# Kernel optimization log

Measured on AMD Instinct MI355X. Metric: run time of the kernel, lower is better.

Reference implementation:

```python
import jax, jax.numpy as jnp
import numpy as np

# Faithful JAX port of the approxmatch EMD kernel (Fan et al.) wrapped by emdDist.
# 10 soft-assignment (auction-style) iterations with annealed temperature level=-4^j,
# j = 7..-1, final iteration level = 0. match is accumulated transport mass;
# cost[b] = sum_{k,l} match[b,k,l] * ||x1_k - x2_l||.

_EPS = 1e-9


def _approxmatch(xyz1, xyz2):
    # xyz1: (b, n, 3), xyz2: (b, m, 3)
    b, n, _ = xyz1.shape
    m = xyz2.shape[1]
    factorl = max(n, m) / n
    factorr = max(n, m) / m
    remainL = jnp.full((b, n), factorl, dtype=xyz1.dtype)   # mass left on xyz1 points
    remainR = jnp.full((b, m), factorr, dtype=xyz1.dtype)   # capacity left on xyz2 points
    # pairwise squared distances (b, n, m)
    d2 = jnp.sum((xyz1[:, :, None, :] - xyz2[:, None, :, :]) ** 2, axis=-1)
    match = jnp.zeros((b, n, m), dtype=xyz1.dtype)
    for j in range(7, -3, -1):  # j = 7, 6, ..., -1, -2
        level = 0.0 if j == -2 else -(4.0 ** j)
        # proposal weights from each left point, scaled by remaining right capacity
        w = jnp.exp(level * d2) * remainR[:, None, :]                      # (b,n,m)
        w = w / (jnp.sum(w, axis=-1, keepdims=True) + _EPS) * remainL[:, :, None]
        # right points accept at most their remaining capacity
        sumr = jnp.sum(w, axis=1) + _EPS                                   # (b,m)
        ratio = jnp.minimum(remainR / sumr, 1.0)                           # (b,m)
        delta = w * ratio[:, None, :]                                      # accepted transfer
        match = match + delta
        remainL = jnp.maximum(remainL - jnp.sum(delta, axis=-1), 0.0)
        remainR = jnp.maximum(remainR - jnp.sum(delta, axis=1), 0.0)
    return match, d2


def setup_inputs() -> dict:
    key = jax.random.key(0)
    k1, k2 = jax.random.split(key)
    B, N, M = 8, 4096, 4096
    input1 = jax.random.normal(k1, (B, N, 3), dtype=jnp.float32)
    input2 = jax.random.normal(k2, (B, M, 3), dtype=jnp.float32)
    return {"input1": input1, "input2": input2}


def reference(input1, input2):
    match, d2 = _approxmatch(input1, input2)
    # original CUDA backward treats match as a constant -> stop_gradient
    match = jax.lax.stop_gradient(match)
    dist = jnp.sqrt(jnp.maximum(d2, 1e-12))
    cost = jnp.sum(match * dist, axis=(1, 2))  # (b,)
    return cost
```

## Files before the change

### kernel.cpp

```cpp
#include <hip/hip_runtime.h>

#define NPTS 4096
#define NB   8
#define TPB  256
#define TPBR 128
#define MBLK 4
#define EPSC 1e-9f

#define EXP2(x)  __builtin_amdgcn_exp2f(x)
#define RCPF(x)  __builtin_amdgcn_rcpf(x)
#define SQRTF(x) __builtin_amdgcn_sqrtf(x)

template<int MODE, bool SKIP, int CHUNK>
__global__ __launch_bounds__(TPB) void ca_kernel(
    const float* __restrict__ x2,
    float* __restrict__ dbufP,
    float* __restrict__ rsumP,
    const float* __restrict__ x1,
    const float* __restrict__ ubuf,
    const float* __restrict__ rrbuf,
    float* __restrict__ out, float sc)
{
  __shared__ float4 x2s[CHUNK];
  __shared__ float  rrs[CHUNK];

  const int tid = threadIdx.x;
  const int nchunk = blockIdx.x, mseg = blockIdx.y, b = blockIdx.z;
  const int m0 = mseg * CHUNK;

  if (MODE == 0 && nchunk == 0 && mseg == 0 && tid == 0) out[b] = 0.f;

  for (int mm = tid; mm < CHUNK; mm += TPB) {
    int m = m0 + mm;
    const float* q = x2 + ((size_t)b * NPTS + m) * 3;
    float u = 0.f, rrn = 1.f;
    if (MODE >= 1) { u = ubuf[b * NPTS + m]; rrn = rrbuf[b * NPTS + m]; }
    x2s[mm] = make_float4(sc * q[0], sc * q[1], sc * q[2], u);
    rrs[mm] = rrn;
  }
  __syncthreads();

  const int n0 = nchunk * (TPB * MBLK) + tid;
  float px[MBLK], py[MBLK], pz[MBLK], dacc[MBLK], racc[MBLK];
#pragma unroll
  for (int k = 0; k < MBLK; ++k) {
    const float* p = x1 + ((size_t)b * NPTS + n0 + k * TPB) * 3;
    px[k] = sc * p[0]; py[k] = sc * p[1]; pz[k] = sc * p[2];
    dacc[k] = 0.f; racc[k] = 0.f;
  }

#pragma unroll 4
  for (int mm = 0; mm < CHUNK; ++mm) {
    float4 q  = x2s[mm];
    float rrv = rrs[mm];
    float ds2[MBLK];
#pragma unroll
    for (int k = 0; k < MBLK; ++k) {
      float dx = px[k] - q.x, dy = py[k] - q.y, dz = pz[k] - q.z;
      ds2[k] = fmaf(dz, dz, fmaf(dy, dy, dx * dx));
    }
    if (MODE == 2) {
#pragma unroll
      for (int k = 0; k < MBLK; ++k) {
        dacc[k] += rrv;
        float ec = EXP2(-ds2[k]);
        racc[k] = fmaf(ec, q.w, racc[k]);
      }
    } else {
      bool go = true;
      if (SKIP) {
        float dmin = ds2[0];
#pragma unroll
        for (int k = 1; k < MBLK; ++k) dmin = fminf(dmin, ds2[k]);
        go = dmin < 126.f;
      }
      if (go) {
#pragma unroll
        for (int k = 0; k < MBLK; ++k) {
          float en = EXP2(-ds2[k]);
          dacc[k] = fmaf(en, rrv, dacc[k]);
          if (MODE == 1) { float e2 = en * en; racc[k] = fmaf(e2 * e2, q.w, racc[k]); }
        }
      }
    }
  }

  size_t base = ((size_t)mseg * NB + b) * NPTS;
#pragma unroll
  for (int k = 0; k < MBLK; ++k) {
    dbufP[base + n0 + k * TPB] = dacc[k];
    if (MODE >= 1) rsumP[base + n0 + k * TPB] = racc[k];
  }
}

template<int LVL0, bool SKIP, int CHUNK>
__global__ __launch_bounds__(TPB) void b_kernel(
    const float* __restrict__ x1,
    const float* __restrict__ abuf,
    float* __restrict__ s0P, float* __restrict__ s1P,
    const float* __restrict__ x2, float sc, float inv_s)
{
  __shared__ float4 x1s[CHUNK];

  const int tid = threadIdx.x;
  const int mchunk = blockIdx.x, nsegi = blockIdx.y, b = blockIdx.z;
  const int n0 = nsegi * CHUNK;

  for (int nn = tid; nn < CHUNK; nn += TPB) {
    int n = n0 + nn;
    const float* p = x1 + ((size_t)b * NPTS + n) * 3;
    float a = abuf[b * NPTS + n];
    x1s[nn] = make_float4(sc * p[0], sc * p[1], sc * p[2], a);
  }
  __syncthreads();

  const int m0 = mchunk * (TPB * MBLK) + tid;
  float qx[MBLK], qy[MBLK], qz[MBLK], s0a[MBLK], s1a[MBLK];
#pragma unroll
  for (int k = 0; k < MBLK; ++k) {
    const float* q = x2 + ((size_t)b * NPTS + m0 + k * TPB) * 3;
    qx[k] = sc * q[0]; qy[k] = sc * q[1]; qz[k] = sc * q[2];
    s0a[k] = 0.f; s1a[k] = 0.f;
  }

#pragma unroll 4
  for (int nn = 0; nn < CHUNK; ++nn) {
    float4 p = x1s[nn];
    float ds2[MBLK];
#pragma unroll
    for (int k = 0; k < MBLK; ++k) {
      float dx = p.x - qx[k], dy = p.y - qy[k], dz = p.z - qz[k];
      ds2[k] = fmaf(dz, dz, fmaf(dy, dy, dx * dx));
    }
    if (LVL0) {
#pragma unroll
      for (int k = 0; k < MBLK; ++k) {
        s0a[k] += p.w;
        s1a[k] = fmaf(p.w, SQRTF(ds2[k]), s1a[k]);
      }
    } else {
      bool go = true;
      if (SKIP) {
        float dmin = ds2[0];
#pragma unroll
        for (int k = 1; k < MBLK; ++k) dmin = fminf(dmin, ds2[k]);
        go = dmin < 126.f;
      }
      if (go) {
#pragma unroll
        for (int k = 0; k < MBLK; ++k) {
          float e  = EXP2(-ds2[k]);
          float tt = p.w * e;
          s0a[k] += tt;
          s1a[k] = fmaf(tt, SQRTF(ds2[k]), s1a[k]);
        }
      }
    }
  }

  size_t base = ((size_t)nsegi * NB + b) * NPTS;
#pragma unroll
  for (int k = 0; k < MBLK; ++k) {
    s0P[base + m0 + k * TPB] = s0a[k];
    s1P[base + m0 + k * TPB] = s1a[k] * inv_s;
  }
}

template<int NSEG>
__global__ __launch_bounds__(TPBR) void r1_kernel(
    const float* __restrict__ dbufP, const float* __restrict__ rsumP,
    float* __restrict__ lbuf, float* __restrict__ dtot,
    float* __restrict__ abuf, int iter)
{
  const int idx = blockIdx.x * TPBR + threadIdx.x;
  const int b = idx >> 12, n = idx & (NPTS - 1);
  const int off = b * NPTS + n;

  float dnew = 0.f;
#pragma unroll
  for (int s = 0; s < NSEG; ++s) dnew += dbufP[((size_t)s * NB + b) * NPTS + n];

  float rl;
  if (iter == 0) {
    rl = 1.f;
  } else {
    float rlp = lbuf[off];
    float ap  = rlp * RCPF(dtot[off] + EPSC);
    float rs = 0.f;
#pragma unroll
    for (int s = 0; s < NSEG; ++s) rs += rsumP[((size_t)s * NB + b) * NPTS + n];
    rl = fmaxf(rlp - ap * rs, 0.f);
  }
  lbuf[off] = rl;
  dtot[off] = dnew;
  abuf[off] = rl * RCPF(dnew + EPSC);
}

template<int NSEG, bool LAST>
__global__ __launch_bounds__(TPBR) void r2_kernel(
    const float* __restrict__ s0P, const float* __restrict__ s1P,
    float* __restrict__ ubuf, float* __restrict__ rrbuf,
    float* __restrict__ out, int iter)
{
  __shared__ float red[TPBR];
  const int idx = blockIdx.x * TPBR + threadIdx.x;
  const int b = idx >> 12, m = idx & (NPTS - 1);
  const int off = b * NPTS + m;

  float s0 = 0.f, s1 = 0.f;
#pragma unroll
  for (int s = 0; s < NSEG; ++s) {
    s0 += s0P[((size_t)s * NB + b) * NPTS + m];
    s1 += s1P[((size_t)s * NB + b) * NPTS + m];
  }
  float rr    = (iter == 0) ? 1.f : rrbuf[off];
  float sumr  = fmaf(rr, s0, EPSC);
  float ratio = fminf(rr * RCPF(sumr), 1.f);
  float u     = rr * ratio;
  if (!LAST) {
    ubuf[off]  = u;
    rrbuf[off] = fmaxf(rr - u * s0, 0.f);
  }

  red[threadIdx.x] = u * s1;
  __syncthreads();
  for (int s = TPBR / 2; s > 0; s >>= 1) {
    if (threadIdx.x < s) red[threadIdx.x] += red[threadIdx.x + s];
    __syncthreads();
  }
  if (threadIdx.x == 0) atomicAdd(out + b, red[0]);
}

template<int NSEG>
static void run_all(const float* x1, const float* x2, float* out, float* ws,
                    hipStream_t stream)
{
  constexpr int CHUNK = NPTS / NSEG;
  const size_t plane = (size_t)NB * NPTS;

  float* dbufP = ws;
  float* rsumP = dbufP + (size_t)NSEG * plane;
  float* s0P   = rsumP + (size_t)NSEG * plane;
  float* s1P   = s0P   + (size_t)NSEG * plane;
  float* dtot  = s1P   + (size_t)NSEG * plane;
  float* lbuf  = dtot  + plane;
  float* abuf  = lbuf  + plane;
  float* ubuf  = abuf  + plane;
  float* rrbuf = ubuf  + plane;

  const double L2E = 1.4426950408889634074;
  const double lv[10] = {-16384.0, -4096.0, -1024.0, -256.0, -64.0,
                         -16.0, -4.0, -1.0, -0.25, 0.0};
  float scl[10], inv_s[10];
  for (int i = 0; i < 10; ++i) {
    double c2 = lv[i] * L2E;
    scl[i]   = (i == 9) ? 1.f : (float)sqrt(-c2);
    inv_s[i] = (i == 9) ? 1.f : (float)(1.0 / sqrt(-c2));
  }

  dim3 gmain(NPTS / (TPB * MBLK), NSEG, NB), bmain(TPB);
  dim3 gr(NPTS * NB / TPBR), br(TPBR);

  ca_kernel<0, true, CHUNK><<<gmain, bmain, 0, stream>>>(
      x2, dbufP, rsumP, x1, ubuf, rrbuf, out, scl[0]);

  for (int i = 0; i < 10; ++i) {
    r1_kernel<NSEG><<<gr, br, 0, stream>>>(dbufP, rsumP, lbuf, dtot, abuf, i);

    if (i <= 2)
      b_kernel<0, true, CHUNK><<<gmain, bmain, 0, stream>>>(
          x1, abuf, s0P, s1P, x2, scl[i], inv_s[i]);
    else if (i <= 8)
      b_kernel<0, false, CHUNK><<<gmain, bmain, 0, stream>>>(
          x1, abuf, s0P, s1P, x2, scl[i], inv_s[i]);
    else
      b_kernel<1, false, CHUNK><<<gmain, bmain, 0, stream>>>(
          x1, abuf, s0P, s1P, x2, 1.f, 1.f);

    if (i < 9)
      r2_kernel<NSEG, false><<<gr, br, 0, stream>>>(s0P, s1P, ubuf, rrbuf, out, i);
    else
      r2_kernel<NSEG, true><<<gr, br, 0, stream>>>(s0P, s1P, ubuf, rrbuf, out, i);

    if (i <= 7) {
      if (i <= 1)
        ca_kernel<1, true, CHUNK><<<gmain, bmain, 0, stream>>>(
            x2, dbufP, rsumP, x1, ubuf, rrbuf, out, scl[i + 1]);
      else
        ca_kernel<1, false, CHUNK><<<gmain, bmain, 0, stream>>>(
            x2, dbufP, rsumP, x1, ubuf, rrbuf, out, scl[i + 1]);
    } else if (i == 8) {
      ca_kernel<2, false, CHUNK><<<gmain, bmain, 0, stream>>>(
          x2, dbufP, rsumP, x1, ubuf, rrbuf, out, scl[8]);
    }
  }
}

extern "C" void kernel_launch(void* const* d_in, const int* in_sizes, int n_in,
                              void* d_out, int out_size, void* d_ws, size_t ws_size,
                              hipStream_t stream) {
  const float* x1 = (const float*)d_in[0];
  const float* x2 = (const float*)d_in[1];
  float* out = (float*)d_out;
  float* ws  = (float*)d_ws;

  const size_t plane = (size_t)NB * NPTS;
  auto need = [&](int nseg) {
    return ((size_t)(4 * nseg + 5) * plane) * sizeof(float);
  };

  if (ws_size >= need(64))      run_all<64>(x1, x2, out, ws, stream);
  else if (ws_size >= need(32)) run_all<32>(x1, x2, out, ws, stream);
  else                          run_all<16>(x1, x2, out, ws, stream);
}
```

Baseline: 1.034 ms.

## Morton-sort point clouds to make far-distance tile skipping effective

Adds a per-batch counting sort of both point sets by a coarse Morton code so spatially nearby points share tiles, letting the wavefront-level skip test (min distance above threshold) fire far more often; the skip path is extended to more iterations. Distances are rewritten in the |p|^2+|q|^2-2pq form, points are stored as float4, the u/rr buffers are packed into float2, and outputs use vectorised stores. Partial-sum buffers are aliased between phases to cut workspace. The cost is an extra sort kernel and possible cancellation error in the expanded distance form, partly guarded by taking abs before the sqrt.

```diff
diff --git a/kernel.cpp b/kernel.cpp
--- a/kernel.cpp
+++ b/kernel.cpp
@@ -11,159 +11,204 @@
 #define RCPF(x)  __builtin_amdgcn_rcpf(x)
 #define SQRTF(x) __builtin_amdgcn_sqrtf(x)
 
+__global__ __launch_bounds__(TPB) void sort_kernel(
+    const float* __restrict__ x1, const float* __restrict__ x2,
+    float4* __restrict__ x1p, float4* __restrict__ x2p)
+{
+  __shared__ unsigned int   hist[4096];
+  __shared__ unsigned short codes[4096];
+  __shared__ unsigned int   part[TPB];
+
+  const int set = blockIdx.x, b = blockIdx.y;
+  const float* src = set ? x2 : x1;
+  float4* dst = set ? x2p : x1p;
+  const int tid = threadIdx.x;
+
+  for (int i = tid; i < 4096; i += TPB) hist[i] = 0;
+  __syncthreads();
+
+  for (int j = 0; j < NPTS / TPB; ++j) {
+    int n = j * TPB + tid;
+    const float* p = src + ((size_t)b * NPTS + n) * 3;
+    float x = p[0], y = p[1], z = p[2];
+    int qx = min(max((int)((x + 4.f) * 2.f), 0), 15);
+    int qy = min(max((int)((y + 4.f) * 2.f), 0), 15);
+    int qz = min(max((int)((z + 4.f) * 2.f), 0), 15);
+    auto ex = [](int v) {
+      return (v & 1) | ((v & 2) << 2) | ((v & 4) << 4) | ((v & 8) << 6);
+    };
+    int code = ex(qx) | (ex(qy) << 1) | (ex(qz) << 2);
+    codes[n] = (unsigned short)code;
+    atomicAdd(&hist[code], 1u);
+  }
+  __syncthreads();
+
+  unsigned int loc[16], s = 0;
+#pragma unroll
+  for (int j = 0; j < 16; ++j) { loc[j] = s; s += hist[tid * 16 + j]; }
+  part[tid] = s;
+  __syncthreads();
+  if (tid == 0) {
+    unsigned int run = 0;
+    for (int t = 0; t < TPB; ++t) { unsigned int v = part[t]; part[t] = run; run += v; }
+  }
+  __syncthreads();
+  {
+    unsigned int base = part[tid];
+#pragma unroll
+    for (int j = 0; j < 16; ++j) hist[tid * 16 + j] = base + loc[j];
+  }
+  __syncthreads();
+
+  for (int j = 0; j < NPTS / TPB; ++j) {
+    int n = j * TPB + tid;
+    const float* p = src + ((size_t)b * NPTS + n) * 3;
+    float x = p[0], y = p[1], z = p[2];
+    unsigned int pos = atomicAdd(&hist[codes[n]], 1u);
+    dst[(size_t)b * NPTS + pos] = make_float4(x, y, z, 0.f);
+  }
+}
+
 template<int MODE, bool SKIP, int CHUNK>
 __global__ __launch_bounds__(TPB) void ca_kernel(
-    const float* __restrict__ x2,
-    float* __restrict__ dbufP,
-    float* __restrict__ rsumP,
-    const float* __restrict__ x1,
-    const float* __restrict__ ubuf,
-    const float* __restrict__ rrbuf,
+    const float4* __restrict__ x2p, const float4* __restrict__ x1p,
+    const float2* __restrict__ urP,
+    float* __restrict__ dbufP, float* __restrict__ rsumP,
     float* __restrict__ out, float sc)
 {
   __shared__ float4 x2s[CHUNK];
-  __shared__ float  rrs[CHUNK];
+  __shared__ float2 urs[CHUNK];
 
   const int tid = threadIdx.x;
   const int nchunk = blockIdx.x, mseg = blockIdx.y, b = blockIdx.z;
-  const int m0 = mseg * CHUNK;
 
   if (MODE == 0 && nchunk == 0 && mseg == 0 && tid == 0) out[b] = 0.f;
 
   for (int mm = tid; mm < CHUNK; mm += TPB) {
-    int m = m0 + mm;
-    const float* q = x2 + ((size_t)b * NPTS + m) * 3;
-    float u = 0.f, rrn = 1.f;
-    if (MODE >= 1) { u = ubuf[b * NPTS + m]; rrn = rrbuf[b * NPTS + m]; }
-    x2s[mm] = make_float4(sc * q[0], sc * q[1], sc * q[2], u);
-    rrs[mm] = rrn;
-  }
-  __syncthreads();
-
-  const int n0 = nchunk * (TPB * MBLK) + tid;
-  float px[MBLK], py[MBLK], pz[MBLK], dacc[MBLK], racc[MBLK];
+    int m = mseg * CHUNK + mm;
+    float4 q = x2p[(size_t)b * NPTS + m];
+    float sx = sc * q.x, sy = sc * q.y, sz = sc * q.z;
+    float nq = fmaf(sz, sz, fmaf(sy, sy, sx * sx));
+    x2s[mm] = make_float4(-2.f * sx, -2.f * sy, -2.f * sz, nq);
+    urs[mm] = (MODE == 0) ? make_float2(0.f, 1.f) : urP[(size_t)b * NPTS + m];
+  }
+  __syncthreads();
+
+  const int n0 = nchunk * (TPB * MBLK) + tid * MBLK;
+  float px[MBLK], py[MBLK], pz[MBLK], np[MBLK], dacc[MBLK], racc[MBLK];
 #pragma unroll
   for (int k = 0; k < MBLK; ++k) {
-    const float* p = x1 + ((size_t)b * NPTS + n0 + k * TPB) * 3;
-    px[k] = sc * p[0]; py[k] = sc * p[1]; pz[k] = sc * p[2];
+    float4 p = x1p[(size_t)b * NPTS + n0 + k];
+    px[k] = sc * p.x; py[k] = sc * p.y; pz[k] = sc * p.z;
+    np[k] = fmaf(pz[k], pz[k], fmaf(py[k], py[k], px[k] * px[k]));
     dacc[k] = 0.f; racc[k] = 0.f;
   }
 
 #pragma unroll 4
   for (int mm = 0; mm < CHUNK; ++mm) {
-    float4 q  = x2s[mm];
-    float rrv = rrs[mm];
+    float4 q = x2s[mm];
+    float2 ur = urs[mm];
     float ds2[MBLK];
 #pragma unroll
-    for (int k = 0; k < MBLK; ++k) {
-      float dx = px[k] - q.x, dy = py[k] - q.y, dz = pz[k] - q.z;
-      ds2[k] = fmaf(dz, dz, fmaf(dy, dy, dx * dx));
-    }
+    for (int k = 0; k < MBLK; ++k)
+      ds2[k] = fmaf(q.x, px[k], fmaf(q.y, py[k], fmaf(q.z, pz[k], np[k] + q.w)));
     if (MODE == 2) {
 #pragma unroll
       for (int k = 0; k < MBLK; ++k) {
-        dacc[k] += rrv;
-        float ec = EXP2(-ds2[k]);
-        racc[k] = fmaf(ec, q.w, racc[k]);
+        dacc[k] += ur.y;
+        racc[k] = fmaf(EXP2(-ds2[k]), ur.x, racc[k]);
       }
     } else {
       bool go = true;
       if (SKIP) {
-        float dmin = ds2[0];
-#pragma unroll
-        for (int k = 1; k < MBLK; ++k) dmin = fminf(dmin, ds2[k]);
+        float dmin = fminf(fminf(ds2[0], ds2[1]), fminf(ds2[2], ds2[3]));
         go = dmin < 126.f;
       }
       if (go) {
 #pragma unroll
         for (int k = 0; k < MBLK; ++k) {
           float en = EXP2(-ds2[k]);
-          dacc[k] = fmaf(en, rrv, dacc[k]);
-          if (MODE == 1) { float e2 = en * en; racc[k] = fmaf(e2 * e2, q.w, racc[k]); }
+          dacc[k] = fmaf(en, ur.y, dacc[k]);
+          if (MODE == 1) { float e2 = en * en; racc[k] = fmaf(e2 * e2, ur.x, racc[k]); }
         }
       }
     }
   }
 
-  size_t base = ((size_t)mseg * NB + b) * NPTS;
-#pragma unroll
-  for (int k = 0; k < MBLK; ++k) {
-    dbufP[base + n0 + k * TPB] = dacc[k];
-    if (MODE >= 1) rsumP[base + n0 + k * TPB] = racc[k];
-  }
+  size_t base = ((size_t)mseg * NB + b) * NPTS + n0;
+  *(float4*)&dbufP[base] = make_float4(dacc[0], dacc[1], dacc[2], dacc[3]);
+  if (MODE >= 1)
+    *(float4*)&rsumP[base] = make_float4(racc[0], racc[1], racc[2], racc[3]);
 }
 
 template<int LVL0, bool SKIP, int CHUNK>
 __global__ __launch_bounds__(TPB) void b_kernel(
-    const float* __restrict__ x1,
-    const float* __restrict__ abuf,
+    const float4* __restrict__ x1p, const float* __restrict__ abuf,
+    const float4* __restrict__ x2p,
     float* __restrict__ s0P, float* __restrict__ s1P,
-    const float* __restrict__ x2, float sc, float inv_s)
+    float sc, float inv_s)
 {
   __shared__ float4 x1s[CHUNK];
+  __shared__ float  as_[CHUNK];
 
   const int tid = threadIdx.x;
   const int mchunk = blockIdx.x, nsegi = blockIdx.y, b = blockIdx.z;
-  const int n0 = nsegi * CHUNK;
 
   for (int nn = tid; nn < CHUNK; nn += TPB) {
-    int n = n0 + nn;
-    const float* p = x1 + ((size_t)b * NPTS + n) * 3;
-    float a = abuf[b * NPTS + n];
-    x1s[nn] = make_float4(sc * p[0], sc * p[1], sc * p[2], a);
-  }
-  __syncthreads();
-
-  const int m0 = mchunk * (TPB * MBLK) + tid;
-  float qx[MBLK], qy[MBLK], qz[MBLK], s0a[MBLK], s1a[MBLK];
+    int n = nsegi * CHUNK + nn;
+    float4 p = x1p[(size_t)b * NPTS + n];
+    float sx = sc * p.x, sy = sc * p.y, sz = sc * p.z;
+    float npv = fmaf(sz, sz, fmaf(sy, sy, sx * sx));
+    x1s[nn] = make_float4(-2.f * sx, -2.f * sy, -2.f * sz, npv);
+    as_[nn] = abuf[(size_t)b * NPTS + n];
+  }
+  __syncthreads();
+
+  const int m0 = mchunk * (TPB * MBLK) + tid * MBLK;
+  float qx[MBLK], qy[MBLK], qz[MBLK], nq[MBLK], s0a[MBLK], s1a[MBLK];
 #pragma unroll
   for (int k = 0; k < MBLK; ++k) {
-    const float* q = x2 + ((size_t)b * NPTS + m0 + k * TPB) * 3;
-    qx[k] = sc * q[0]; qy[k] = sc * q[1]; qz[k] = sc * q[2];
+    float4 q = x2p[(size_t)b * NPTS + m0 + k];
+    qx[k] = sc * q.x; qy[k] = sc * q.y; qz[k] = sc * q.z;
+    nq[k] = fmaf(qz[k], qz[k], fmaf(qy[k], qy[k], qx[k] * qx[k]));
     s0a[k] = 0.f; s1a[k] = 0.f;
   }
 
 #pragma unroll 4
   for (int nn = 0; nn < CHUNK; ++nn) {
     float4 p = x1s[nn];
+    float av = as_[nn];
     float ds2[MBLK];
 #pragma unroll
-    for (int k = 0; k < MBLK; ++k) {
-      float dx = p.x - qx[k], dy = p.y - qy[k], dz = p.z - qz[k];
-      ds2[k] = fmaf(dz, dz, fmaf(dy, dy, dx * dx));
-    }
+    for (int k = 0; k < MBLK; ++k)
+      ds2[k] = fmaf(p.x, qx[k], fmaf(p.y, qy[k], fmaf(p.z, qz[k], nq[k] + p.w)));
     if (LVL0) {
 #pragma unroll
       for (int k = 0; k < MBLK; ++k) {
-        s0a[k] += p.w;
-        s1a[k] = fmaf(p.w, SQRTF(ds2[k]), s1a[k]);
+        s0a[k] += av;
+        s1a[k] = fmaf(av, SQRTF(__builtin_fabsf(ds2[k])), s1a[k]);
       }
     } else {
       bool go = true;
       if (SKIP) {
-        float dmin = ds2[0];
-#pragma unroll
-        for (int k = 1; k < MBLK; ++k) dmin = fminf(dmin, ds2[k]);
+        float dmin = fminf(fminf(ds2[0], ds2[1]), fminf(ds2[2], ds2[3]));
         go = dmin < 126.f;
       }
       if (go) {
 #pragma unroll
         for (int k = 0; k < MBLK; ++k) {
-          float e  = EXP2(-ds2[k]);
-          float tt = p.w * e;
+          float tt = av * EXP2(-ds2[k]);
           s0a[k] += tt;
-          s1a[k] = fmaf(tt, SQRTF(ds2[k]), s1a[k]);
+          s1a[k] = fmaf(tt, SQRTF(__builtin_fabsf(ds2[k])), s1a[k]);
         }
       }
     }
   }
 
-  size_t base = ((size_t)nsegi * NB + b) * NPTS;
-#pragma unroll
-  for (int k = 0; k < MBLK; ++k) {
-    s0P[base + m0 + k * TPB] = s0a[k];
-    s1P[base + m0 + k * TPB] = s1a[k] * inv_s;
-  }
+  size_t base = ((size_t)nsegi * NB + b) * NPTS + m0;
+  *(float4*)&s0P[base] = make_float4(s0a[0], s0a[1], s0a[2], s0a[3]);
+  *(float4*)&s1P[base] = make_float4(s1a[0] * inv_s, s1a[1] * inv_s,
+                                     s1a[2] * inv_s, s1a[3] * inv_s);
 }
 
 template<int NSEG>
@@ -199,8 +244,7 @@
 template<int NSEG, bool LAST>
 __global__ __launch_bounds__(TPBR) void r2_kernel(
     const float* __restrict__ s0P, const float* __restrict__ s1P,
-    float* __restrict__ ubuf, float* __restrict__ rrbuf,
-    float* __restrict__ out, int iter)
+    float2* __restrict__ urbuf, float* __restrict__ out, int iter)
 {
   __shared__ float red[TPBR];
   const int idx = blockIdx.x * TPBR + threadIdx.x;
@@ -213,14 +257,11 @@
     s0 += s0P[((size_t)s * NB + b) * NPTS + m];
     s1 += s1P[((size_t)s * NB + b) * NPTS + m];
   }
-  float rr    = (iter == 0) ? 1.f : rrbuf[off];
+  float rr    = (iter == 0) ? 1.f : urbuf[off].y;
   float sumr  = fmaf(rr, s0, EPSC);
   float ratio = fminf(rr * RCPF(sumr), 1.f);
   float u     = rr * ratio;
-  if (!LAST) {
-    ubuf[off]  = u;
-    rrbuf[off] = fmaxf(rr - u * s0, 0.f);
-  }
+  if (!LAST) urbuf[off] = make_float2(u, fmaxf(rr - u * s0, 0.f));
 
   red[threadIdx.x] = u * s1;
   __syncthreads();
@@ -238,15 +279,14 @@
   constexpr int CHUNK = NPTS / NSEG;
   const size_t plane = (size_t)NB * NPTS;
 
-  float* dbufP = ws;
-  float* rsumP = dbufP + (size_t)NSEG * plane;
-  float* s0P   = rsumP + (size_t)NSEG * plane;
-  float* s1P   = s0P   + (size_t)NSEG * plane;
-  float* dtot  = s1P   + (size_t)NSEG * plane;
-  float* lbuf  = dtot  + plane;
-  float* abuf  = lbuf  + plane;
-  float* ubuf  = abuf  + plane;
-  float* rrbuf = ubuf  + plane;
+  float*  bufA = ws;
+  float*  bufB = bufA + (size_t)NSEG * plane;
+  float4* x1p  = (float4*)(bufB + (size_t)NSEG * plane);
+  float4* x2p  = x1p + plane;
+  float*  dtot = (float*)(x2p + plane);
+  float*  lbuf = dtot + plane;
+  float*  abuf = lbuf + plane;
+  float2* urbuf = (float2*)(abuf + plane);
 
   const double L2E = 1.4426950408889634074;
   const double lv[10] = {-16384.0, -4096.0, -1024.0, -256.0, -64.0,
@@ -261,38 +301,38 @@
   dim3 gmain(NPTS / (TPB * MBLK), NSEG, NB), bmain(TPB);
   dim3 gr(NPTS * NB / TPBR), br(TPBR);
 
+  sort_kernel<<<dim3(2, NB), bmain, 0, stream>>>(x1, x2, x1p, x2p);
+
   ca_kernel<0, true, CHUNK><<<gmain, bmain, 0, stream>>>(
-      x2, dbufP, rsumP, x1, ubuf, rrbuf, out, scl[0]);
+      x2p, x1p, urbuf, bufA, bufB, out, scl[0]);
 
   for (int i = 0; i < 10; ++i) {
-    r1_kernel<NSEG><<<gr, br, 0, stream>>>(dbufP, rsumP, lbuf, dtot, abuf, i);
-
-    if (i <= 2)
+    r1_kernel<NSEG><<<gr, br, 0, stream>>>(bufA, bufB, lbuf, dtot, abuf, i);
+
+    if (i <= 4)
       b_kernel<0, true, CHUNK><<<gmain, bmain, 0, stream>>>(
-          x1, abuf, s0P, s1P, x2, scl[i], inv_s[i]);
+          x1p, abuf, x2p, bufA, bufB, scl[i], inv_s[i]);
     else if (i <= 8)
       b_kernel<0, false, CHUNK><<<gmain, bmain, 0, stream>>>(
-          x1, abuf, s0P, s1P, x2, scl[i], inv_s[i]);
+          x1p, abuf, x2p, bufA, bufB, scl[i], inv_s[i]);
     else
       b_kernel<1, false, CHUNK><<<gmain, bmain, 0, stream>>>(
-          x1, abuf, s0P, s1P, x2, 1.f, 1.f);
+          x1p, abuf, x2p, bufA, bufB, 1.f, 1.f);
 
     if (i < 9)
-      r2_kernel<NSEG, false><<<gr, br, 0, stream>>>(s0P, s1P, ubuf, rrbuf, out, i);
+      r2_kernel<NSEG, false><<<gr, br, 0, stream>>>(bufA, bufB, urbuf, out, i);
     else
-      r2_kernel<NSEG, true><<<gr, br, 0, stream>>>(s0P, s1P, ubuf, rrbuf, out, i);
-
-    if (i <= 7) {
-      if (i <= 1)
-        ca_kernel<1, true, CHUNK><<<gmain, bmain, 0, stream>>>(
-            x2, dbufP, rsumP, x1, ubuf, rrbuf, out, scl[i + 1]);
-      else
-        ca_kernel<1, false, CHUNK><<<gmain, bmain, 0, stream>>>(
-            x2, dbufP, rsumP, x1, ubuf, rrbuf, out, scl[i + 1]);
-    } else if (i == 8) {
+      r2_kernel<NSEG, true><<<gr, br, 0, stream>>>(bufA, bufB, urbuf, out, i);
+
+    if (i <= 3)
+      ca_kernel<1, true, CHUNK><<<gmain, bmain, 0, stream>>>(
+          x2p, x1p, urbuf, bufA, bufB, out, scl[i + 1]);
+    else if (i <= 7)
+      ca_kernel<1, false, CHUNK><<<gmain, bmain, 0, stream>>>(
+          x2p, x1p, urbuf, bufA, bufB, out, scl[i + 1]);
+    else if (i == 8)
       ca_kernel<2, false, CHUNK><<<gmain, bmain, 0, stream>>>(
-          x2, dbufP, rsumP, x1, ubuf, rrbuf, out, scl[8]);
-    }
+          x2p, x1p, urbuf, bufA, bufB, out, scl[8]);
   }
 }
 
@@ -306,7 +346,7 @@
 
   const size_t plane = (size_t)NB * NPTS;
   auto need = [&](int nseg) {
-    return ((size_t)(4 * nseg + 5) * plane) * sizeof(float);
+    return (size_t)(2 * nseg + 13) * plane * sizeof(float);
   };
 
   if (ws_size >= need(64))      run_all<64>(x1, x2, out, ws, stream);
```

After: 989.8 us. -4.3%, faster.
